# Kernel optimization log

Measured on AMD Instinct MI355X. Metric: run time of the kernel, lower is better.

The kernel has to match this reference:

```python
import jax, jax.numpy as jnp
import numpy as np

FEATURE_MAPS = (38, 19, 10, 5, 3, 1)
BOXES_PER_LOC = (4, 6, 6, 6, 4, 4)
IMAGE_SIZE = 300
DEC_SIZE = 64  # WhatDecoder output resolution
MAX_OBJECTS = 10
Z_WHAT = 64


def _recon_indices():
    # Maps per-prior slots (8732) to per-location slots (1940), matching
    # Decoder.reconstruction_indices: each location index repeated boxes_per_loc times.
    idx, last = [], 0
    for fm, bpl in zip(FEATURE_MAPS, BOXES_PER_LOC):
        loc = np.arange(fm * fm) + last
        idx.append(np.repeat(loc, bpl))
        last = loc[-1] + 1
    return jnp.asarray(np.concatenate(idx), dtype=jnp.int32)


def _deconv2x2(x, W, b):
    # ConvTranspose2d(kernel=2, stride=2): each input pixel expands to a 2x2 block.
    n, c, h, w = x.shape
    o = W.shape[1]
    y = jnp.einsum('nchw,coab->nohawb', x, W).reshape(n, o, 2 * h, 2 * w)
    return y + b[None, :, None, None]


def _what_decoder(z, params):
    # z (M, Z_WHAT) -> (M, 3, 64, 64) in [0,1]
    x = z[:, :, None, None]
    nl = len(params)
    for i, (W, b) in enumerate(params):
        x = _deconv2x2(x, W, b)
        x = jax.nn.relu(x) if i < nl - 1 else jax.nn.sigmoid(x)
    return x


def _stn(images, z_where):
    # Spatial transformer: place (M,3,S,S) glyphs into IMAGE_SIZE canvas at box
    # z_where (M,4) = (cx,cy,w,h) in [0,1]; bilinear sampling, zeros padding.
    M, _, S, _ = images.shape
    cx, cy, w, h = (z_where[:, i] for i in range(4))
    # output pixel centers in normalized [-1,1] coords (align_corners=False)
    coords = (2.0 * jnp.arange(IMAGE_SIZE, dtype=images.dtype) + 1.0) / IMAGE_SIZE - 1.0
    xo = coords[None, None, :]
    yo = coords[None, :, None]
    eps = 1e-6
    u = (xo - (2.0 * cx - 1.0)[:, None, None]) / (w[:, None, None] + eps)  # (M,H,W)
    v = (yo - (2.0 * cy - 1.0)[:, None, None]) / (h[:, None, None] + eps)
    ix = ((u + 1.0) * S - 1.0) / 2.0  # input pixel coords
    iy = ((v + 1.0) * S - 1.0) / 2.0

    def sample_one(img, iy, ix):
        iy0 = jnp.floor(iy)
        ix0 = jnp.floor(ix)
        wy1 = iy - iy0
        wx1 = ix - ix0
        wy0 = 1.0 - wy1
        wx0 = 1.0 - wx1

        def g(y, x):
            yi = jnp.clip(y, 0, S - 1).astype(jnp.int32)
            xi = jnp.clip(x, 0, S - 1).astype(jnp.int32)
            valid = ((y >= 0) & (y < S) & (x >= 0) & (x < S)).astype(img.dtype)
            return img[:, yi, xi] * valid  # (3,H,W)

        return (g(iy0, ix0) * wy0 * wx0 + g(iy0, ix0 + 1) * wy0 * wx1
                + g(iy0 + 1, ix0) * wy1 * wx0 + g(iy0 + 1, ix0 + 1) * wy1 * wx1)

    return jax.vmap(sample_one)(images, iy, ix)  # (M,3,H,H)


def setup_inputs() -> dict:
    key = jax.random.key(0)
    ks = jax.random.split(key, 20)
    B, NLOC, NPRI = 16, 1940, 8732
    chans = (Z_WHAT, 256, 128, 64, 32, 16, 3)
    inp = {
        'z_what': jax.random.normal(ks[0], (B, NLOC, Z_WHAT), jnp.float32),
        'z_where': jax.random.uniform(ks[1], (B, NPRI, 4), jnp.float32),
        'z_present': jax.random.randint(ks[2], (B, NPRI, 1), 0, 2, jnp.int32),
        'z_depth': jax.random.normal(ks[3], (B, NLOC, 1), jnp.float32),
    }
    for i in range(6):
        ci, co = chans[i], chans[i + 1]
        inp[f'W{i}'] = jax.random.normal(ks[4 + i], (ci, co, 2, 2), jnp.float32) * 0.1
        inp[f'b{i}'] = jnp.zeros((co,), jnp.float32)
    return inp


def reference(z_what, z_where, z_present, z_depth,
              W0, b0, W1, b1, W2, b2, W3, b3, W4, b4, W5, b5):
    params = [(W0, b0), (W1, b1), (W2, b2), (W3, b3), (W4, b4), (W5, b5)]
    idx = _recon_indices()
    zw = z_what[:, idx]      # (B, P, D) ragged location->prior gather
    zd = z_depth[:, idx, 0]  # (B, P)
    order = jnp.argsort(-zd, axis=1)[:, :MAX_OBJECTS]  # depth sort, descending
    B, K = order.shape

    def gat(t):
        return jnp.take_along_axis(
            t, jnp.broadcast_to(order[:, :, None], (B, K, t.shape[-1])), axis=1)

    sw = gat(zw)            # (B,K,D)
    swr = gat(z_where)      # (B,K,4)
    sp = gat(z_present)     # (B,K,1)

    decoded = _what_decoder(sw.reshape(B * K, Z_WHAT), params)      # (B*K,3,64,64)
    transformed = _stn(decoded, swr.reshape(B * K, 4))              # (B*K,3,300,300)
    present = (sp == 1).astype(transformed.dtype).reshape(B * K, 1, 1, 1)
    objs = (transformed * present).reshape(B, K, 3, IMAGE_SIZE, IMAGE_SIZE)

    # z-buffer merge: per pixel, take first nonzero object in depth order
    nz = objs != 0.0
    first = nz & (jnp.cumsum(nz.astype(jnp.int32), axis=1) == 1)
    return jnp.sum(objs * first.astype(objs.dtype), axis=1)  # (B,3,300,300)
```

## Files before the change

### kernel.cpp

```cpp
#include <hip/hip_runtime.h>
#include <cmath>

#define NLOC 1940
#define NPRI 8732
#define BATCH 16
#define KOBJ 10

__device__ __forceinline__ void ins3(float v, int i,
    float& a0, float& a1, float& a2, int& j0, int& j1, int& j2)
{
    if (v > a0 || (v == a0 && i < j0)) { a2=a1; j2=j1; a1=a0; j1=j0; a0=v; j0=i; }
    else if (v > a1 || (v == a1 && i < j1)) { a2=a1; j2=j1; a1=v; j1=i; }
    else if (v > a2 || (v == a2 && i < j2)) { a2=v; j2=i; }
}

__global__ __launch_bounds__(256) void prep_kernel(
    const float* __restrict__ W0, const float* __restrict__ W1, float* __restrict__ Wr,
    const float* __restrict__ z_what, const float* __restrict__ z_where,
    const int* __restrict__ z_present, const float* __restrict__ z_depth,
    float* __restrict__ gathered, float* __restrict__ paramsF, int* __restrict__ paramsI)
{
    __shared__ float sv[768];
    __shared__ int   si[768];
    __shared__ int   locs3[3];
    const int tid = threadIdx.x;

    if (blockIdx.x < 768) {
        const int idx = blockIdx.x * 256 + tid;
        if (idx < 65536) {
            int q = idx >> 14, rem = idx & 16383, c = rem >> 8, o = rem & 255;
            Wr[idx] = W0[(((c << 8) | o) << 2) + q];
        } else {
            int i2 = idx - 65536;
            int q = i2 >> 15, rem = i2 & 32767, c = rem >> 7, o = rem & 127;
            Wr[idx] = W1[(((c << 7) | o) << 2) + q];
        }
        return;
    }

    const int b = blockIdx.x - 768;
    float v0 = -INFINITY, v1 = -INFINITY, v2 = -INFINITY;
    int   i0 = NLOC, i1 = NLOC, i2 = NLOC;
    for (int i = tid; i < NLOC; i += 256) {
        float v = z_depth[b * NLOC + i];
        ins3(v, i, v0, v1, v2, i0, i1, i2);
    }
    sv[tid*3+0] = v0; sv[tid*3+1] = v1; sv[tid*3+2] = v2;
    si[tid*3+0] = i0; si[tid*3+1] = i1; si[tid*3+2] = i2;
    __syncthreads();
    for (int s = 128; s > 0; s >>= 1) {
        if (tid < s) {
            float a0 = sv[tid*3], a1 = sv[tid*3+1], a2 = sv[tid*3+2];
            int   j0 = si[tid*3], j1 = si[tid*3+1], j2 = si[tid*3+2];
            const int o = tid + s;
            ins3(sv[o*3+0], si[o*3+0], a0, a1, a2, j0, j1, j2);
            ins3(sv[o*3+1], si[o*3+1], a0, a1, a2, j0, j1, j2);
            ins3(sv[o*3+2], si[o*3+2], a0, a1, a2, j0, j1, j2);
            sv[tid*3] = a0; sv[tid*3+1] = a1; sv[tid*3+2] = a2;
            si[tid*3] = j0; si[tid*3+1] = j1; si[tid*3+2] = j2;
        }
        __syncthreads();
    }

    if (tid == 0) {
        int cnt = 0, taken = 0;
        for (int j = 0; j < 3; ++j) {
            int L = si[j];
            locs3[j] = L;
            if (taken >= KOBJ) continue;
            int start, bpl;
            if (L < 1444)      { start = 4 * L;                 bpl = 4; }
            else if (L < 1805) { start = 5776 + 6 * (L - 1444); bpl = 6; }
            else if (L < 1905) { start = 7942 + 6 * (L - 1805); bpl = 6; }
            else if (L < 1930) { start = 8542 + 6 * (L - 1905); bpl = 6; }
            else if (L < 1939) { start = 8692 + 4 * (L - 1930); bpl = 4; }
            else               { start = 8728;                  bpl = 4; }
            for (int o = 0; o < bpl && taken < KOBJ; ++o, ++taken) {
                int p = start + o;
                if (z_present[b * NPRI + p] == 1) {
                    const float* zw = z_where + (b * NPRI + p) * 4;
                    float cx = zw[0], cy = zw[1], w_ = zw[2], h_ = zw[3];
                    float* pf = paramsF + (b * KOBJ + cnt) * 4;
                    pf[0] = __fadd_rn(w_, 1e-6f);
                    pf[1] = __fadd_rn(h_, 1e-6f);
                    pf[2] = __fsub_rn(__fmul_rn(2.0f, cx), 1.0f);
                    pf[3] = __fsub_rn(__fmul_rn(2.0f, cy), 1.0f);
                    paramsI[b * 12 + 2 + cnt] = b * 3 + j;
                    cnt++;
                }
            }
        }
        paramsI[b * 12] = cnt;
    }
    __syncthreads();
    if (tid < 192) {
        int j = tid >> 6, c = tid & 63;
        gathered[(b * 3 + j) * 64 + c] = z_what[(b * NLOC + locs3[j]) * 64 + c];
    }
}

__global__ __launch_bounds__(256) void dec_fused(
    const float* __restrict__ gathered, const float* __restrict__ Wr,
    const float* __restrict__ b0v, const float* __restrict__ b1v,
    const float* __restrict__ W2, const float* __restrict__ b2v,
    const float* __restrict__ W3, const float* __restrict__ b3v,
    const float* __restrict__ W4, const float* __restrict__ b4v,
    const float* __restrict__ W5, const float* __restrict__ b5v,
    float* __restrict__ decoded)
{
    __shared__ __align__(16) float P[4096];
    __shared__ __align__(16) float Q[2048];
    __shared__ __align__(16) float Zs[256];
    const int r  = blockIdx.x;
    const int g  = blockIdx.y;
    const int t  = threadIdx.x;
    const int y1 = r >> 2, x1 = r & 3;
    const int q0 = (y1 >> 1) * 2 + (x1 >> 1);
    const int p1 = (y1 & 1) * 2 + (x1 & 1);
    const int s4 = g * 4;

    Zs[t] = gathered[(s4 + (t & 3)) * 64 + (t >> 2)];
    __syncthreads();

    {
        const float* w0 = Wr + q0 * 16384 + t;
        float bv = b0v[t];
        float4 acc = make_float4(bv, bv, bv, bv);
        #pragma unroll 8
        for (int c = 0; c < 64; ++c) {
            float w = w0[c << 8];
            float4 xs = *reinterpret_cast<const float4*>(Zs + (c << 2));
            acc.x = fmaf(xs.x, w, acc.x); acc.y = fmaf(xs.y, w, acc.y);
            acc.z = fmaf(xs.z, w, acc.z); acc.w = fmaf(xs.w, w, acc.w);
        }
        *reinterpret_cast<float4*>(P + (t << 2)) =
            make_float4(fmaxf(acc.x, 0.f), fmaxf(acc.y, 0.f), fmaxf(acc.z, 0.f), fmaxf(acc.w, 0.f));
    }
    __syncthreads();

    {
        const int o = t & 127, h = t >> 7;
        const float* w1 = Wr + 65536 + p1 * 32768 + o;
        float4 acc;
        if (h == 0) { float bv = b1v[o]; acc = make_float4(bv, bv, bv, bv); }
        else        { acc = make_float4(0.f, 0.f, 0.f, 0.f); }
        const int cb = h << 7;
        #pragma unroll 8
        for (int c = 0; c < 128; ++c) {
            float w = w1[(cb + c) << 7];
            float4 xs = *reinterpret_cast<const float4*>(P + ((cb + c) << 2));
            acc.x = fmaf(xs.x, w, acc.x); acc.y = fmaf(xs.y, w, acc.y);
            acc.z = fmaf(xs.z, w, acc.z); acc.w = fmaf(xs.w, w, acc.w);
        }
        if (h == 1) *reinterpret_cast<float4*>(P + 1024 + (o << 2)) = acc;
        __syncthreads();
        if (h == 0) {
            float4 p2 = *reinterpret_cast<const float4*>(P + 1024 + (o << 2));
            acc.x += p2.x; acc.y += p2.y; acc.z += p2.z; acc.w += p2.w;
            *reinterpret_cast<float4*>(Q + (o << 2)) =
                make_float4(fmaxf(acc.x, 0.f), fmaxf(acc.y, 0.f), fmaxf(acc.z, 0.f), fmaxf(acc.w, 0.f));
        }
    }
    __syncthreads();

    {
        const float* w2 = W2 + t;
        float bv = b2v[t >> 2];
        float4 acc = make_float4(bv, bv, bv, bv);
        #pragma unroll 8
        for (int ci = 0; ci < 128; ++ci) {
            float w = w2[ci << 8];
            float4 xs = *reinterpret_cast<const float4*>(Q + (ci << 2));
            acc.x = fmaf(xs.x, w, acc.x); acc.y = fmaf(xs.y, w, acc.y);
            acc.z = fmaf(xs.z, w, acc.z); acc.w = fmaf(xs.w, w, acc.w);
        }
        *reinterpret_cast<float4*>(P + (t << 2)) =
            make_float4(fmaxf(acc.x, 0.f), fmaxf(acc.y, 0.f), fmaxf(acc.z, 0.f), fmaxf(acc.w, 0.f));
    }
    __syncthreads();

    {
        const int px = t & 15, coa = t >> 4;
        const int ly = px >> 2, lx = px & 3;
        const int par = (ly >> 1) * 2 + (lx >> 1);
        const int wp  = (ly & 1) * 2 + (lx & 1);
        const float* w3 = W3 + coa * 4 + wp;
        float bva = b3v[coa], bvb = b3v[coa + 16];
        float4 a0 = make_float4(bva, bva, bva, bva);
        float4 a1 = make_float4(bvb, bvb, bvb, bvb);
        #pragma unroll 4
        for (int ci = 0; ci < 64; ++ci) {
            float4 xs = *reinterpret_cast<const float4*>(P + (ci << 4) + (par << 2));
            float wa = w3[ci << 7];
            float wb = w3[(ci << 7) + 64];
            a0.x = fmaf(xs.x, wa, a0.x); a0.y = fmaf(xs.y, wa, a0.y);
            a0.z = fmaf(xs.z, wa, a0.z); a0.w = fmaf(xs.w, wa, a0.w);
            a1.x = fmaf(xs.x, wb, a1.x); a1.y = fmaf(xs.y, wb, a1.y);
            a1.z = fmaf(xs.z, wb, a1.z); a1.w = fmaf(xs.w, wb, a1.w);
        }
        *reinterpret_cast<float4*>(Q + (coa << 6) + (px << 2)) =
            make_float4(fmaxf(a0.x, 0.f), fmaxf(a0.y, 0.f), fmaxf(a0.z, 0.f), fmaxf(a0.w, 0.f));
        *reinterpret_cast<float4*>(Q + ((coa + 16) << 6) + (px << 2)) =
            make_float4(fmaxf(a1.x, 0.f), fmaxf(a1.y, 0.f), fmaxf(a1.z, 0.f), fmaxf(a1.w, 0.f));
    }
    __syncthreads();

    {
        const int px = t & 63, co0 = t >> 6;
        const int ly = px >> 3, lx = px & 7;
        const int par = (ly >> 1) * 4 + (lx >> 1);
        const int wp  = (ly & 1) * 2 + (lx & 1);
        const float* w4 = W4 + co0 * 4 + wp;
        float4 acc[4];
        #pragma unroll
        for (int k = 0; k < 4; ++k) {
            float bv = b4v[co0 + 4 * k];
            acc[k] = make_float4(bv, bv, bv, bv);
        }
        #pragma unroll 4
        for (int ci = 0; ci < 32; ++ci) {
            float4 xs = *reinterpret_cast<const float4*>(Q + (ci << 6) + (par << 2));
            #pragma unroll
            for (int k = 0; k < 4; ++k) {
                float w = w4[(ci << 6) + k * 16];
                acc[k].x = fmaf(xs.x, w, acc[k].x); acc[k].y = fmaf(xs.y, w, acc[k].y);
                acc[k].z = fmaf(xs.z, w, acc[k].z); acc[k].w = fmaf(xs.w, w, acc[k].w);
            }
        }
        #pragma unroll
        for (int k = 0; k < 4; ++k) {
            *reinterpret_cast<float4*>(P + ((co0 + 4 * k) << 8) + (px << 2)) =
                make_float4(fmaxf(acc[k].x, 0.f), fmaxf(acc[k].y, 0.f),
                            fmaxf(acc[k].z, 0.f), fmaxf(acc[k].w, 0.f));
        }
    }
    __syncthreads();

    {
        const int px = t;
        const int ly = px >> 4, lx = px & 15;
        const int par = (ly >> 1) * 8 + (lx >> 1);
        const int wp  = (ly & 1) * 2 + (lx & 1);
        const int gy = y1 * 16 + ly, gx = x1 * 16 + lx;
        const float* w5 = W5 + wp;
        float4 acc[3];
        #pragma unroll
        for (int c = 0; c < 3; ++c) {
            float bv = b5v[c];
            acc[c] = make_float4(bv, bv, bv, bv);
        }
        #pragma unroll 4
        for (int ci = 0; ci < 16; ++ci) {
            float4 xs = *reinterpret_cast<const float4*>(P + (ci << 8) + (par << 2));
            #pragma unroll
            for (int c = 0; c < 3; ++c) {
                float w = w5[ci * 12 + c * 4];
                acc[c].x = fmaf(xs.x, w, acc[c].x); acc[c].y = fmaf(xs.y, w, acc[c].y);
                acc[c].z = fmaf(xs.z, w, acc[c].z); acc[c].w = fmaf(xs.w, w, acc[c].w);
            }
        }
        const int pbase = (gy * 64 + gx) * 3;
        #pragma unroll
        for (int c = 0; c < 3; ++c) {
            float vs[4] = {acc[c].x, acc[c].y, acc[c].z, acc[c].w};
            #pragma unroll
            for (int s = 0; s < 4; ++s)
                decoded[(s4 + s) * 12288 + pbase + c] = 1.0f / (1.0f + expf(-vs[s]));
        }
    }
}

__global__ __launch_bounds__(256) void stn_kernel(
    const float* __restrict__ decoded, const float* __restrict__ paramsF,
    const int* __restrict__ paramsI, float* __restrict__ out)
{
    const int b = blockIdx.y;
    const int pix0 = blockIdx.x * 256;
    const int yfirst = pix0 / 300;
    __shared__ float sp[KOBJ][4];
    __shared__ int   ssamp[KOBJ];
    __shared__ int   scnt;
    __shared__ float s_wy0[KOBJ][2], s_wy1[KOBJ][2];
    __shared__ int   s_rb0[KOBJ][2], s_rb1[KOBJ][2];
    __shared__ unsigned char s_cov[KOBJ][2];
    __shared__ unsigned char s_vy[KOBJ][2];
    __shared__ int s_list[KOBJ];
    __shared__ int s_lc;
    const int tid = threadIdx.x;

    if (tid == 0) scnt = paramsI[b * 12];
    if (tid < KOBJ) {
        #pragma unroll
        for (int c = 0; c < 4; ++c) sp[tid][c] = paramsF[(b * KOBJ + tid) * 4 + c];
        ssamp[tid] = paramsI[b * 12 + 2 + tid];
    }
    __syncthreads();

    if (tid < 2 * scnt) {
        const int k = tid >> 1, sel = tid & 1;
        int yy = yfirst + sel; if (yy > 299) yy = 299;
        const float yo = __fsub_rn(__fdiv_rn(__fadd_rn(__fmul_rn(2.0f, (float)yy), 1.0f), 300.0f), 1.0f);
        const float v  = __fdiv_rn(__fsub_rn(yo, sp[k][3]), sp[k][1]);
        const float iy = __fmul_rn(__fsub_rn(__fmul_rn(__fadd_rn(v, 1.0f), 64.0f), 1.0f), 0.5f);
        const bool cov = (iy > -1.0f && iy < 64.0f);
        s_cov[k][sel] = cov ? 1 : 0;
        const float iy0f = floorf(iy);
        const float iy1f = __fadd_rn(iy0f, 1.0f);
        const float wy1  = __fsub_rn(iy, iy0f);
        s_wy1[k][sel] = wy1;
        s_wy0[k][sel] = __fsub_rn(1.0f, wy1);
        const bool vy0 = (iy0f >= 0.0f) && (iy0f < 64.0f);
        const bool vy1 = (iy1f >= 0.0f) && (iy1f < 64.0f);
        s_vy[k][sel] = (unsigned char)((vy0 ? 1 : 0) | (vy1 ? 2 : 0));
        s_rb0[k][sel] = ((int)fminf(fmaxf(iy0f, 0.0f), 63.0f)) * 64;
        s_rb1[k][sel] = ((int)fminf(fmaxf(iy1f, 0.0f), 63.0f)) * 64;
    }
    __syncthreads();
    if (tid == 0) {
        int lc = 0;
        for (int k = 0; k < scnt; ++k)
            if (s_cov[k][0] | s_cov[k][1]) s_list[lc++] = k;
        s_lc = lc;
    }
    __syncthreads();

    const int pix = pix0 + tid;
    if (pix < 90000) {
        const int y = pix / 300;
        const int x = pix - y * 300;
        const int rs = y - yfirst;
        const float xo = __fsub_rn(__fdiv_rn(__fadd_rn(__fmul_rn(2.0f, (float)x), 1.0f), 300.0f), 1.0f);

        float o0 = 0.0f, o1 = 0.0f, o2 = 0.0f;
        bool d0 = false, d1 = false, d2 = false;
        const int lc = s_lc;
        for (int m = 0; m < lc; ++m) {
            const int k = s_list[m];
            if (!s_cov[k][rs]) continue;
            const float u  = __fdiv_rn(__fsub_rn(xo, sp[k][2]), sp[k][0]);
            const float ix = __fmul_rn(__fsub_rn(__fmul_rn(__fadd_rn(u, 1.0f), 64.0f), 1.0f), 0.5f);
            if (!(ix > -1.0f && ix < 64.0f)) continue;

            const float ix0f = floorf(ix);
            const float ix1f = __fadd_rn(ix0f, 1.0f);
            const float wx1 = __fsub_rn(ix, ix0f);
            const float wx0 = __fsub_rn(1.0f, wx1);
            const bool vx0 = (ix0f >= 0.0f) && (ix0f < 64.0f);
            const bool vx1 = (ix1f >= 0.0f) && (ix1f < 64.0f);
            const int x0 = (int)fminf(fmaxf(ix0f, 0.0f), 63.0f);
            const int x1 = (int)fminf(fmaxf(ix1f, 0.0f), 63.0f);

            const float wy0 = s_wy0[k][rs], wy1 = s_wy1[k][rs];
            const int rb0 = s_rb0[k][rs], rb1 = s_rb1[k][rs];
            const unsigned char vy = s_vy[k][rs];
            const bool m00 = (vy & 1) && vx0, m01 = (vy & 1) && vx1;
            const bool m10 = (vy & 2) && vx0, m11 = (vy & 2) && vx1;
            const float* img = decoded + ssamp[k] * 12288;

            float g00x = 0.f, g00y = 0.f, g00z = 0.f;
            float g01x = 0.f, g01y = 0.f, g01z = 0.f;
            float g10x = 0.f, g10y = 0.f, g10z = 0.f;
            float g11x = 0.f, g11y = 0.f, g11z = 0.f;
            if (m00) { const float* p = img + (rb0 + x0) * 3; g00x = p[0]; g00y = p[1]; g00z = p[2]; }
            if (m01) { const float* p = img + (rb0 + x1) * 3; g01x = p[0]; g01y = p[1]; g01z = p[2]; }
            if (m10) { const float* p = img + (rb1 + x0) * 3; g10x = p[0]; g10y = p[1]; g10z = p[2]; }
            if (m11) { const float* p = img + (rb1 + x1) * 3; g11x = p[0]; g11y = p[1]; g11z = p[2]; }

            if (!d0) {
                float val = g00x * wy0 * wx0 + g01x * wy0 * wx1 + g10x * wy1 * wx0 + g11x * wy1 * wx1;
                if (val != 0.0f) { o0 = val; d0 = true; }
            }
            if (!d1) {
                float val = g00y * wy0 * wx0 + g01y * wy0 * wx1 + g10y * wy1 * wx0 + g11y * wy1 * wx1;
                if (val != 0.0f) { o1 = val; d1 = true; }
            }
            if (!d2) {
                float val = g00z * wy0 * wx0 + g01z * wy0 * wx1 + g10z * wy1 * wx0 + g11z * wy1 * wx1;
                if (val != 0.0f) { o2 = val; d2 = true; }
            }
            if (d0 && d1 && d2) break;
        }
        const int ob = b * 270000 + pix;
        out[ob] = o0;
        out[ob + 90000] = o1;
        out[ob + 180000] = o2;
    }
}

extern "C" void kernel_launch(void* const* d_in, const int* in_sizes, int n_in,
                              void* d_out, int out_size, void* d_ws, size_t ws_size,
                              hipStream_t stream)
{
    const float* z_what    = (const float*)d_in[0];
    const float* z_where   = (const float*)d_in[1];
    const int*   z_present = (const int*)d_in[2];
    const float* z_depth   = (const float*)d_in[3];
    const float* W0 = (const float*)d_in[4];   const float* b0 = (const float*)d_in[5];
    const float* W1 = (const float*)d_in[6];   const float* b1 = (const float*)d_in[7];
    const float* W2 = (const float*)d_in[8];   const float* b2 = (const float*)d_in[9];
    const float* W3 = (const float*)d_in[10];  const float* b3 = (const float*)d_in[11];
    const float* W4 = (const float*)d_in[12];  const float* b4 = (const float*)d_in[13];
    const float* W5 = (const float*)d_in[14];  const float* b5 = (const float*)d_in[15];

    float* ws = (float*)d_ws;
    float* gathered = ws;
    float* paramsF  = ws + 16384;
    int*   paramsI  = (int*)(ws + 17408);
    float* decoded  = ws + 32768;
    float* Wr       = (float*)d_out;
    float* outp     = (float*)d_out;

    hipLaunchKernelGGL(prep_kernel, dim3(784), dim3(256), 0, stream,
                       W0, W1, Wr, z_what, z_where, z_present, z_depth,
                       gathered, paramsF, paramsI);
    hipLaunchKernelGGL(dec_fused, dim3(16, 12), dim3(256), 0, stream,
                       gathered, Wr, b0, b1, W2, b2, W3, b3, W4, b4, W5, b5, decoded);
    hipLaunchKernelGGL(stn_kernel, dim3(352, BATCH), dim3(256), 0, stream,
                       decoded, paramsF, paramsI, outp);
}
```

Measured before the change: 150.5 us.

## Precompute per-object pixel bounds and halve decoder samples per block

```diff
diff --git a/kernel.cpp b/kernel.cpp
--- a/kernel.cpp
+++ b/kernel.cpp
@@ -14,15 +14,27 @@
     else if (v > a2 || (v == a2 && i < j2)) { a2=v; j2=i; }
 }
 
+__device__ __forceinline__ float ix_chain(int x, float shift, float wh) {
+    const float xo = __fsub_rn(__fdiv_rn(__fadd_rn(__fmul_rn(2.0f, (float)x), 1.0f), 300.0f), 1.0f);
+    const float u  = __fdiv_rn(__fsub_rn(xo, shift), wh);
+    return __fmul_rn(__fsub_rn(__fmul_rn(__fadd_rn(u, 1.0f), 64.0f), 1.0f), 0.5f);
+}
+
 __global__ __launch_bounds__(256) void prep_kernel(
     const float* __restrict__ W0, const float* __restrict__ W1, float* __restrict__ Wr,
     const float* __restrict__ z_what, const float* __restrict__ z_where,
     const int* __restrict__ z_present, const float* __restrict__ z_depth,
-    float* __restrict__ gathered, float* __restrict__ paramsF, int* __restrict__ paramsI)
+    float* __restrict__ gathered, float* __restrict__ paramsF, int* __restrict__ paramsI,
+    int* __restrict__ obnd)
 {
     __shared__ float sv[768];
     __shared__ int   si[768];
     __shared__ int   locs3[3];
+    __shared__ int   sj_start[3], sj_bpl[3];
+    __shared__ int   spres[10], sjj[10];
+    __shared__ float szw[10][4];
+    __shared__ float lpf[KOBJ][4];
+    __shared__ int   lcnt;
     const int tid = threadIdx.x;
 
     if (blockIdx.x < 768) {
@@ -62,37 +74,71 @@
         __syncthreads();
     }
 
+    if (tid < 3) {
+        int L = si[tid];
+        locs3[tid] = L;
+        int start, bpl;
+        if (L < 1444)      { start = 4 * L;                 bpl = 4; }
+        else if (L < 1805) { start = 5776 + 6 * (L - 1444); bpl = 6; }
+        else if (L < 1905) { start = 7942 + 6 * (L - 1805); bpl = 6; }
+        else if (L < 1930) { start = 8542 + 6 * (L - 1905); bpl = 6; }
+        else if (L < 1939) { start = 8692 + 4 * (L - 1930); bpl = 4; }
+        else               { start = 8728;                  bpl = 4; }
+        sj_start[tid] = start; sj_bpl[tid] = bpl;
+    }
+    __syncthreads();
+    if (tid < 10) {
+        const int b0 = sj_bpl[0], b1 = sj_bpl[1];
+        int j, o;
+        if (tid < b0)           { j = 0; o = tid; }
+        else if (tid < b0 + b1) { j = 1; o = tid - b0; }
+        else                    { j = 2; o = tid - b0 - b1; }
+        const int p = sj_start[j] + o;
+        sjj[tid]   = j;
+        spres[tid] = z_present[b * NPRI + p];
+        const float4 zw = *reinterpret_cast<const float4*>(z_where + (b * NPRI + p) * 4);
+        szw[tid][0] = zw.x; szw[tid][1] = zw.y; szw[tid][2] = zw.z; szw[tid][3] = zw.w;
+    }
+    __syncthreads();
     if (tid == 0) {
-        int cnt = 0, taken = 0;
-        for (int j = 0; j < 3; ++j) {
-            int L = si[j];
-            locs3[j] = L;
-            if (taken >= KOBJ) continue;
-            int start, bpl;
-            if (L < 1444)      { start = 4 * L;                 bpl = 4; }
-            else if (L < 1805) { start = 5776 + 6 * (L - 1444); bpl = 6; }
-            else if (L < 1905) { start = 7942 + 6 * (L - 1805); bpl = 6; }
-            else if (L < 1930) { start = 8542 + 6 * (L - 1905); bpl = 6; }
-            else if (L < 1939) { start = 8692 + 4 * (L - 1930); bpl = 4; }
-            else               { start = 8728;                  bpl = 4; }
-            for (int o = 0; o < bpl && taken < KOBJ; ++o, ++taken) {
-                int p = start + o;
-                if (z_present[b * NPRI + p] == 1) {
-                    const float* zw = z_where + (b * NPRI + p) * 4;
-                    float cx = zw[0], cy = zw[1], w_ = zw[2], h_ = zw[3];
-                    float* pf = paramsF + (b * KOBJ + cnt) * 4;
-                    pf[0] = __fadd_rn(w_, 1e-6f);
-                    pf[1] = __fadd_rn(h_, 1e-6f);
-                    pf[2] = __fsub_rn(__fmul_rn(2.0f, cx), 1.0f);
-                    pf[3] = __fsub_rn(__fmul_rn(2.0f, cy), 1.0f);
-                    paramsI[b * 12 + 2 + cnt] = b * 3 + j;
-                    cnt++;
-                }
+        int cnt = 0;
+        for (int i = 0; i < 10; ++i) {
+            if (spres[i] == 1) {
+                float p0 = __fadd_rn(szw[i][2], 1e-6f);
+                float p1 = __fadd_rn(szw[i][3], 1e-6f);
+                float p2 = __fsub_rn(__fmul_rn(2.0f, szw[i][0]), 1.0f);
+                float p3 = __fsub_rn(__fmul_rn(2.0f, szw[i][1]), 1.0f);
+                float* pf = paramsF + (b * KOBJ + cnt) * 4;
+                pf[0] = p0; pf[1] = p1; pf[2] = p2; pf[3] = p3;
+                lpf[cnt][0] = p0; lpf[cnt][1] = p1; lpf[cnt][2] = p2; lpf[cnt][3] = p3;
+                paramsI[b * 12 + 2 + cnt] = b * 3 + sjj[i];
+                cnt++;
             }
         }
         paramsI[b * 12] = cnt;
-    }
-    __syncthreads();
+        lcnt = cnt;
+    }
+    __syncthreads();
+    if (tid < 4 * KOBJ) {
+        const int k = tid >> 2, ty = tid & 3;
+        if (k < lcnt) {
+            const float wh = (ty < 2) ? lpf[k][0] : lpf[k][1];
+            const float sh = (ty < 2) ? lpf[k][2] : lpf[k][3];
+            int res;
+            if ((ty & 1) == 0) {
+                int lo = 0, hi = 300;
+                while (lo < hi) { int m = (lo + hi) >> 1;
+                    if (ix_chain(m, sh, wh) > -1.0f) hi = m; else lo = m + 1; }
+                res = lo;
+            } else {
+                int lo = -1, hi = 299;
+                while (lo < hi) { int m = (lo + hi + 1) >> 1;
+                    if (ix_chain(m, sh, wh) < 64.0f) lo = m; else hi = m - 1; }
+                res = lo;
+            }
+            obnd[(b * KOBJ + k) * 4 + ty] = res;
+        }
+    }
     if (tid < 192) {
         int j = tid >> 6, c = tid & 63;
         gathered[(b * 3 + j) * 64 + c] = z_what[(b * NLOC + locs3[j]) * 64 + c];
@@ -108,57 +154,55 @@
     const float* __restrict__ W5, const float* __restrict__ b5v,
     float* __restrict__ decoded)
 {
-    __shared__ __align__(16) float P[4096];
-    __shared__ __align__(16) float Q[2048];
-    __shared__ __align__(16) float Zs[256];
+    __shared__ __align__(16) float P[2048];
+    __shared__ __align__(16) float Q[1024];
+    __shared__ __align__(16) float Zs[128];
     const int r  = blockIdx.x;
     const int g  = blockIdx.y;
     const int t  = threadIdx.x;
     const int y1 = r >> 2, x1 = r & 3;
     const int q0 = (y1 >> 1) * 2 + (x1 >> 1);
     const int p1 = (y1 & 1) * 2 + (x1 & 1);
-    const int s4 = g * 4;
-
-    Zs[t] = gathered[(s4 + (t & 3)) * 64 + (t >> 2)];
+    const int s2 = g * 2;
+
+    if (t < 128) Zs[t] = gathered[(s2 + (t & 1)) * 64 + (t >> 1)];
     __syncthreads();
 
     {
         const float* w0 = Wr + q0 * 16384 + t;
         float bv = b0v[t];
-        float4 acc = make_float4(bv, bv, bv, bv);
+        float2 acc = make_float2(bv, bv);
         #pragma unroll 8
         for (int c = 0; c < 64; ++c) {
             float w = w0[c << 8];
-            float4 xs = *reinterpret_cast<const float4*>(Zs + (c << 2));
+            float2 xs = *reinterpret_cast<const float2*>(Zs + (c << 1));
             acc.x = fmaf(xs.x, w, acc.x); acc.y = fmaf(xs.y, w, acc.y);
-            acc.z = fmaf(xs.z, w, acc.z); acc.w = fmaf(xs.w, w, acc.w);
-        }
-        *reinterpret_cast<float4*>(P + (t << 2)) =
-            make_float4(fmaxf(acc.x, 0.f), fmaxf(acc.y, 0.f), fmaxf(acc.z, 0.f), fmaxf(acc.w, 0.f));
+        }
+        *reinterpret_cast<float2*>(P + (t << 1)) =
+            make_float2(fmaxf(acc.x, 0.f), fmaxf(acc.y, 0.f));
     }
     __syncthreads();
 
     {
         const int o = t & 127, h = t >> 7;
         const float* w1 = Wr + 65536 + p1 * 32768 + o;
-        float4 acc;
-        if (h == 0) { float bv = b1v[o]; acc = make_float4(bv, bv, bv, bv); }
-        else        { acc = make_float4(0.f, 0.f, 0.f, 0.f); }
+        float2 acc;
+        if (h == 0) { float bv = b1v[o]; acc = make_float2(bv, bv); }
+        else        { acc = make_float2(0.f, 0.f); }
         const int cb = h << 7;
         #pragma unroll 8
         for (int c = 0; c < 128; ++c) {
             float w = w1[(cb + c) << 7];
-            float4 xs = *reinterpret_cast<const float4*>(P + ((cb + c) << 2));
+            float2 xs = *reinterpret_cast<const float2*>(P + ((cb + c) << 1));
             acc.x = fmaf(xs.x, w, acc.x); acc.y = fmaf(xs.y, w, acc.y);
-            acc.z = fmaf(xs.z, w, acc.z); acc.w = fmaf(xs.w, w, acc.w);
-        }
-        if (h == 1) *reinterpret_cast<float4*>(P + 1024 + (o << 2)) = acc;
+        }
+        if (h == 1) *reinterpret_cast<float2*>(P + 512 + (o << 1)) = acc;
         __syncthreads();
         if (h == 0) {
-            float4 p2 = *reinterpret_cast<const float4*>(P + 1024 + (o << 2));
-            acc.x += p2.x; acc.y += p2.y; acc.z += p2.z; acc.w += p2.w;
-            *reinterpret_cast<float4*>(Q + (o << 2)) =
-                make_float4(fmaxf(acc.x, 0.f), fmaxf(acc.y, 0.f), fmaxf(acc.z, 0.f), fmaxf(acc.w, 0.f));
+            float2 p2 = *reinterpret_cast<const float2*>(P + 512 + (o << 1));
+            acc.x += p2.x; acc.y += p2.y;
+            *reinterpret_cast<float2*>(Q + (o << 1)) =
+                make_float2(fmaxf(acc.x, 0.f), fmaxf(acc.y, 0.f));
         }
     }
     __syncthreads();
@@ -166,16 +210,15 @@
     {
         const float* w2 = W2 + t;
         float bv = b2v[t >> 2];
-        float4 acc = make_float4(bv, bv, bv, bv);
+        float2 acc = make_float2(bv, bv);
         #pragma unroll 8
         for (int ci = 0; ci < 128; ++ci) {
             float w = w2[ci << 8];
-            float4 xs = *reinterpret_cast<const float4*>(Q + (ci << 2));
+            float2 xs = *reinterpret_cast<const float2*>(Q + (ci << 1));
             acc.x = fmaf(xs.x, w, acc.x); acc.y = fmaf(xs.y, w, acc.y);
-            acc.z = fmaf(xs.z, w, acc.z); acc.w = fmaf(xs.w, w, acc.w);
-        }
-        *reinterpret_cast<float4*>(P + (t << 2)) =
-            make_float4(fmaxf(acc.x, 0.f), fmaxf(acc.y, 0.f), fmaxf(acc.z, 0.f), fmaxf(acc.w, 0.f));
+        }
+        *reinterpret_cast<float2*>(P + (t << 1)) =
+            make_float2(fmaxf(acc.x, 0.f), fmaxf(acc.y, 0.f));
     }
     __syncthreads();
 
@@ -186,22 +229,20 @@
         const int wp  = (ly & 1) * 2 + (lx & 1);
         const float* w3 = W3 + coa * 4 + wp;
         float bva = b3v[coa], bvb = b3v[coa + 16];
-        float4 a0 = make_float4(bva, bva, bva, bva);
-        float4 a1 = make_float4(bvb, bvb, bvb, bvb);
-        #pragma unroll 4
+        float2 a0 = make_float2(bva, bva);
+        float2 a1 = make_float2(bvb, bvb);
+        #pragma unroll 8
         for (int ci = 0; ci < 64; ++ci) {
-            float4 xs = *reinterpret_cast<const float4*>(P + (ci << 4) + (par << 2));
+            float2 xs = *reinterpret_cast<const float2*>(P + (ci << 3) + (par << 1));
             float wa = w3[ci << 7];
             float wb = w3[(ci << 7) + 64];
             a0.x = fmaf(xs.x, wa, a0.x); a0.y = fmaf(xs.y, wa, a0.y);
-            a0.z = fmaf(xs.z, wa, a0.z); a0.w = fmaf(xs.w, wa, a0.w);
             a1.x = fmaf(xs.x, wb, a1.x); a1.y = fmaf(xs.y, wb, a1.y);
-            a1.z = fmaf(xs.z, wb, a1.z); a1.w = fmaf(xs.w, wb, a1.w);
-        }
-        *reinterpret_cast<float4*>(Q + (coa << 6) + (px << 2)) =
-            make_float4(fmaxf(a0.x, 0.f), fmaxf(a0.y, 0.f), fmaxf(a0.z, 0.f), fmaxf(a0.w, 0.f));
-        *reinterpret_cast<float4*>(Q + ((coa + 16) << 6) + (px << 2)) =
-            make_float4(fmaxf(a1.x, 0.f), fmaxf(a1.y, 0.f), fmaxf(a1.z, 0.f), fmaxf(a1.w, 0.f));
+        }
+        *reinterpret_cast<float2*>(Q + (coa << 5) + (px << 1)) =
+            make_float2(fmaxf(a0.x, 0.f), fmaxf(a0.y, 0.f));
+        *reinterpret_cast<float2*>(Q + ((coa + 16) << 5) + (px << 1)) =
+            make_float2(fmaxf(a1.x, 0.f), fmaxf(a1.y, 0.f));
     }
     __syncthreads();
 
@@ -211,28 +252,22 @@
         const int par = (ly >> 1) * 4 + (lx >> 1);
         const int wp  = (ly & 1) * 2 + (lx & 1);
         const float* w4 = W4 + co0 * 4 + wp;
-        float4 acc[4];
+        float2 acc[4];
         #pragma unroll
-        for (int k = 0; k < 4; ++k) {
-            float bv = b4v[co0 + 4 * k];
-            acc[k] = make_float4(bv, bv, bv, bv);
-        }
+        for (int k = 0; k < 4; ++k) { float bv = b4v[co0 + 4 * k]; acc[k] = make_float2(bv, bv); }
         #pragma unroll 4
         for (int ci = 0; ci < 32; ++ci) {
-            float4 xs = *reinterpret_cast<const float4*>(Q + (ci << 6) + (par << 2));
+            float2 xs = *reinterpret_cast<const float2*>(Q + (ci << 5) + (par << 1));
             #pragma unroll
             for (int k = 0; k < 4; ++k) {
                 float w = w4[(ci << 6) + k * 16];
                 acc[k].x = fmaf(xs.x, w, acc[k].x); acc[k].y = fmaf(xs.y, w, acc[k].y);
-                acc[k].z = fmaf(xs.z, w, acc[k].z); acc[k].w = fmaf(xs.w, w, acc[k].w);
             }
         }
         #pragma unroll
-        for (int k = 0; k < 4; ++k) {
-            *reinterpret_cast<float4*>(P + ((co0 + 4 * k) << 8) + (px << 2)) =
-                make_float4(fmaxf(acc[k].x, 0.f), fmaxf(acc[k].y, 0.f),
-                            fmaxf(acc[k].z, 0.f), fmaxf(acc[k].w, 0.f));
-        }
+        for (int k = 0; k < 4; ++k)
+            *reinterpret_cast<float2*>(P + ((co0 + 4 * k) << 7) + (px << 1)) =
+                make_float2(fmaxf(acc[k].x, 0.f), fmaxf(acc[k].y, 0.f));
     }
     __syncthreads();
 
@@ -243,42 +278,38 @@
         const int wp  = (ly & 1) * 2 + (lx & 1);
         const int gy = y1 * 16 + ly, gx = x1 * 16 + lx;
         const float* w5 = W5 + wp;
-        float4 acc[3];
+        float2 acc[3];
         #pragma unroll
-        for (int c = 0; c < 3; ++c) {
-            float bv = b5v[c];
-            acc[c] = make_float4(bv, bv, bv, bv);
-        }
+        for (int c = 0; c < 3; ++c) { float bv = b5v[c]; acc[c] = make_float2(bv, bv); }
         #pragma unroll 4
         for (int ci = 0; ci < 16; ++ci) {
-            float4 xs = *reinterpret_cast<const float4*>(P + (ci << 8) + (par << 2));
+            float2 xs = *reinterpret_cast<const float2*>(P + (ci << 7) + (par << 1));
             #pragma unroll
             for (int c = 0; c < 3; ++c) {
                 float w = w5[ci * 12 + c * 4];
                 acc[c].x = fmaf(xs.x, w, acc[c].x); acc[c].y = fmaf(xs.y, w, acc[c].y);
-                acc[c].z = fmaf(xs.z, w, acc[c].z); acc[c].w = fmaf(xs.w, w, acc[c].w);
             }
         }
         const int pbase = (gy * 64 + gx) * 3;
         #pragma unroll
         for (int c = 0; c < 3; ++c) {
-            float vs[4] = {acc[c].x, acc[c].y, acc[c].z, acc[c].w};
-            #pragma unroll
-            for (int s = 0; s < 4; ++s)
-                decoded[(s4 + s) * 12288 + pbase + c] = 1.0f / (1.0f + expf(-vs[s]));
+            decoded[(s2 + 0) * 12288 + pbase + c] = 1.0f / (1.0f + expf(-acc[c].x));
+            decoded[(s2 + 1) * 12288 + pbase + c] = 1.0f / (1.0f + expf(-acc[c].y));
         }
     }
 }
 
 __global__ __launch_bounds__(256) void stn_kernel(
     const float* __restrict__ decoded, const float* __restrict__ paramsF,
-    const int* __restrict__ paramsI, float* __restrict__ out)
+    const int* __restrict__ paramsI, const int* __restrict__ obnd,
+    float* __restrict__ out)
 {
     const int b = blockIdx.y;
     const int pix0 = blockIdx.x * 256;
     const int yfirst = pix0 / 300;
     __shared__ float sp[KOBJ][4];
     __shared__ int   ssamp[KOBJ];
+    __shared__ int   s_xlo[KOBJ], s_xhi[KOBJ], s_ylo[KOBJ], s_yhi[KOBJ];
     __shared__ int   scnt;
     __shared__ float s_wy0[KOBJ][2], s_wy1[KOBJ][2];
     __shared__ int   s_rb0[KOBJ][2], s_rb1[KOBJ][2];
@@ -293,27 +324,29 @@
         #pragma unroll
         for (int c = 0; c < 4; ++c) sp[tid][c] = paramsF[(b * KOBJ + tid) * 4 + c];
         ssamp[tid] = paramsI[b * 12 + 2 + tid];
+        const int4 bd = *reinterpret_cast<const int4*>(obnd + (b * KOBJ + tid) * 4);
+        s_xlo[tid] = bd.x; s_xhi[tid] = bd.y; s_ylo[tid] = bd.z; s_yhi[tid] = bd.w;
     }
     __syncthreads();
 
     if (tid < 2 * scnt) {
         const int k = tid >> 1, sel = tid & 1;
         int yy = yfirst + sel; if (yy > 299) yy = 299;
-        const float yo = __fsub_rn(__fdiv_rn(__fadd_rn(__fmul_rn(2.0f, (float)yy), 1.0f), 300.0f), 1.0f);
-        const float v  = __fdiv_rn(__fsub_rn(yo, sp[k][3]), sp[k][1]);
-        const float iy = __fmul_rn(__fsub_rn(__fmul_rn(__fadd_rn(v, 1.0f), 64.0f), 1.0f), 0.5f);
-        const bool cov = (iy > -1.0f && iy < 64.0f);
+        const bool cov = (yy >= s_ylo[k]) && (yy <= s_yhi[k]);
         s_cov[k][sel] = cov ? 1 : 0;
-        const float iy0f = floorf(iy);
-        const float iy1f = __fadd_rn(iy0f, 1.0f);
-        const float wy1  = __fsub_rn(iy, iy0f);
-        s_wy1[k][sel] = wy1;
-        s_wy0[k][sel] = __fsub_rn(1.0f, wy1);
-        const bool vy0 = (iy0f >= 0.0f) && (iy0f < 64.0f);
-        const bool vy1 = (iy1f >= 0.0f) && (iy1f < 64.0f);
-        s_vy[k][sel] = (unsigned char)((vy0 ? 1 : 0) | (vy1 ? 2 : 0));
-        s_rb0[k][sel] = ((int)fminf(fmaxf(iy0f, 0.0f), 63.0f)) * 64;
-        s_rb1[k][sel] = ((int)fminf(fmaxf(iy1f, 0.0f), 63.0f)) * 64;
+        if (cov) {
+            const float iy = ix_chain(yy, sp[k][3], sp[k][1]);
+            const float iy0f = floorf(iy);
+            const float iy1f = __fadd_rn(iy0f, 1.0f);
+            const float wy1  = __fsub_rn(iy, iy0f);
+            s_wy1[k][sel] = wy1;
+            s_wy0[k][sel] = __fsub_rn(1.0f, wy1);
+            const bool vy0 = (iy0f >= 0.0f) && (iy0f < 64.0f);
+            const bool vy1 = (iy1f >= 0.0f) && (iy1f < 64.0f);
+            s_vy[k][sel] = (unsigned char)((vy0 ? 1 : 0) | (vy1 ? 2 : 0));
+            s_rb0[k][sel] = ((int)fminf(fmaxf(iy0f, 0.0f), 63.0f)) * 64;
+            s_rb1[k][sel] = ((int)fminf(fmaxf(iy1f, 0.0f), 63.0f)) * 64;
+        }
     }
     __syncthreads();
     if (tid == 0) {
@@ -329,18 +362,15 @@
         const int y = pix / 300;
         const int x = pix - y * 300;
         const int rs = y - yfirst;
-        const float xo = __fsub_rn(__fdiv_rn(__fadd_rn(__fmul_rn(2.0f, (float)x), 1.0f), 300.0f), 1.0f);
-
         float o0 = 0.0f, o1 = 0.0f, o2 = 0.0f;
         bool d0 = false, d1 = false, d2 = false;
         const int lc = s_lc;
         for (int m = 0; m < lc; ++m) {
             const int k = s_list[m];
             if (!s_cov[k][rs]) continue;
-            const float u  = __fdiv_rn(__fsub_rn(xo, sp[k][2]), sp[k][0]);
-            const float ix = __fmul_rn(__fsub_rn(__fmul_rn(__fadd_rn(u, 1.0f), 64.0f), 1.0f), 0.5f);
-            if (!(ix > -1.0f && ix < 64.0f)) continue;
-
+            if (x < s_xlo[k] || x > s_xhi[k]) continue;
+
+            const float ix = ix_chain(x, sp[k][2], sp[k][0]);
             const float ix0f = floorf(ix);
             const float ix1f = __fadd_rn(ix0f, 1.0f);
             const float wx1 = __fsub_rn(ix, ix0f);
@@ -406,15 +436,16 @@
     float* gathered = ws;
     float* paramsF  = ws + 16384;
     int*   paramsI  = (int*)(ws + 17408);
+    int*   obnd     = (int*)(ws + 17664);
     float* decoded  = ws + 32768;
     float* Wr       = (float*)d_out;
     float* outp     = (float*)d_out;
 
     hipLaunchKernelGGL(prep_kernel, dim3(784), dim3(256), 0, stream,
                        W0, W1, Wr, z_what, z_where, z_present, z_depth,
-                       gathered, paramsF, paramsI);
-    hipLaunchKernelGGL(dec_fused, dim3(16, 12), dim3(256), 0, stream,
+                       gathered, paramsF, paramsI, obnd);
+    hipLaunchKernelGGL(dec_fused, dim3(16, 24), dim3(256), 0, stream,
                        gathered, Wr, b0, b1, W2, b2, W3, b3, W4, b4, W5, b5, decoded);
     hipLaunchKernelGGL(stn_kernel, dim3(352, BATCH), dim3(256), 0, stream,
-                       decoded, paramsF, paramsI, outp);
-}
+                       decoded, paramsF, paramsI, obnd, outp);
+}
```

Measured after the change: 148.9 us. Within noise of the previous version (-1.1%).
